# Kernel optimization log

Measured on AMD Instinct MI355X. Metric: run time of the kernel, lower is better.

## Reference

```python
import jax, jax.numpy as jnp
import numpy as np

N, IN_DIM, H1, H2 = 12288, 512, 256, 128

def setup_inputs() -> dict:
    key = jax.random.key(0)
    k = jax.random.split(key, 6)
    glorot = lambda kk, fi, fo: jax.random.normal(kk, (fi, fo), jnp.float32) * np.sqrt(2.0 / (fi + fo))
    return {
        "X": jax.random.normal(k[0], (N, IN_DIM), jnp.float32),
        "adj": jax.random.uniform(k[1], (N, N), jnp.float32) / N,  # scaled like a normalized adjacency
        "noise": jax.random.normal(k[2], (N, H2), jnp.float32),
        "W0": glorot(k[3], IN_DIM, H1),
        "W_mu": glorot(k[4], H1, H2),
        "W_logstd": glorot(k[5], H1, H2),
    }

def reference(X, adj, noise, W0, W_mu, W_logstd):
    # GraphConvSparse layer 1: relu(adj @ (X @ W0))
    hidden = jax.nn.relu(adj @ (X @ W0))            # [N, H1]
    # mean / logstd heads (identity activation)
    mean = adj @ (hidden @ W_mu)                    # [N, H2]
    logstd = adj @ (hidden @ W_logstd)              # [N, H2]
    # reparameterization
    Z = noise * jnp.exp(logstd) + mean              # [N, H2]
    # dot-product decode
    A_pred = jax.nn.sigmoid(Z @ Z.T)                # [N, N]
    return A_pred
```

## Files before the change

kernel.cpp:

```cpp
#include <hip/hip_runtime.h>
#include <stdint.h>

#define NN 12288
#define IND 512
#define H1D 256
#define H2D 128

using bf16x8 = __attribute__((ext_vector_type(8))) short;
using f32x4  = __attribute__((ext_vector_type(4))) float;

__device__ __forceinline__ unsigned short f2bf(float f){
  unsigned int u = __float_as_uint(f);
  return (unsigned short)((u + 0x7fffu + ((u >> 16) & 1u)) >> 16);
}
__device__ __forceinline__ float bf2f(unsigned short h){
  return __uint_as_float(((unsigned int)h) << 16);
}
__device__ __forceinline__ void gload_lds16(const void* g, void* l){
  __builtin_amdgcn_global_load_lds(
      (const __attribute__((address_space(1))) unsigned int*)(uintptr_t)g,
      (__attribute__((address_space(3))) unsigned int*)(unsigned int)(uintptr_t)l,
      16, 0, 0);
}

__global__ __launch_bounds__(256) void k_xw0(const float* __restrict__ X,
                                             const float* __restrict__ W0,
                                             unsigned short* __restrict__ XW0T){
  __shared__ float XsT[32][68];
  __shared__ float Ws[32][36];
  const int t  = (int)threadIdx.x;
  const int n0 = (int)blockIdx.x * 64;
  const int h0 = (int)blockIdx.y * 32;
  const int xr = t >> 2, xc = (t & 3) * 8;
  const int h  = t >> 3, ng = t & 7;
  float acc[8];
#pragma unroll
  for (int j = 0; j < 8; ++j) acc[j] = 0.f;

  for (int k0 = 0; k0 < IND; k0 += 32){
    {
      const float* xp = X + (size_t)(n0 + xr) * IND + k0 + xc;
      float4 a = *(const float4*)xp;
      float4 b = *(const float4*)(xp + 4);
      XsT[xc+0][xr]=a.x; XsT[xc+1][xr]=a.y; XsT[xc+2][xr]=a.z; XsT[xc+3][xr]=a.w;
      XsT[xc+4][xr]=b.x; XsT[xc+5][xr]=b.y; XsT[xc+6][xr]=b.z; XsT[xc+7][xr]=b.w;
    }
    if (t < 128){
      const float* wp = W0 + (size_t)(k0 + xr) * H1D + h0 + xc;
      float4 a = *(const float4*)wp;
      float4 b = *(const float4*)(wp + 4);
      Ws[xr][xc+0]=a.x; Ws[xr][xc+1]=a.y; Ws[xr][xc+2]=a.z; Ws[xr][xc+3]=a.w;
      Ws[xr][xc+4]=b.x; Ws[xr][xc+5]=b.y; Ws[xr][xc+6]=b.z; Ws[xr][xc+7]=b.w;
    }
    __syncthreads();
#pragma unroll 8
    for (int kk = 0; kk < 32; ++kk){
      float wv = Ws[kk][h];
      const float4 x0 = *(const float4*)&XsT[kk][ng*8];
      const float4 x1 = *(const float4*)&XsT[kk][ng*8+4];
      acc[0] += x0.x*wv; acc[1] += x0.y*wv; acc[2] += x0.z*wv; acc[3] += x0.w*wv;
      acc[4] += x1.x*wv; acc[5] += x1.y*wv; acc[6] += x1.z*wv; acc[7] += x1.w*wv;
    }
    __syncthreads();
  }
  uint4 pk;
  pk.x = (unsigned)f2bf(acc[0]) | ((unsigned)f2bf(acc[1]) << 16);
  pk.y = (unsigned)f2bf(acc[2]) | ((unsigned)f2bf(acc[3]) << 16);
  pk.z = (unsigned)f2bf(acc[4]) | ((unsigned)f2bf(acc[5]) << 16);
  pk.w = (unsigned)f2bf(acc[6]) | ((unsigned)f2bf(acc[7]) << 16);
  *(uint4*)(XW0T + (size_t)(h0 + h) * NN + n0 + ng*8) = pk;
}

__global__ __launch_bounds__(512, 4) void k_gemm_adj(const float* __restrict__ A,
                                                     const unsigned short* __restrict__ Bt,
                                                     float* __restrict__ part){
  __shared__ unsigned short Alds[2][48*64];
  __shared__ unsigned short Blds[2][256*64];
  const int t = (int)threadIdx.x;
  const int w = t >> 6, l = t & 63;
  const int l15 = l & 15, l16 = l >> 4;
  const int m0 = (int)blockIdx.x * 48;
  const int khalf = (int)blockIdx.y;
  const int kbase = khalf * 6144;
  const size_t kbyte = (size_t)kbase * 2;

  f32x4 acc[3][2];
#pragma unroll
  for (int mi = 0; mi < 3; ++mi)
#pragma unroll
    for (int ni = 0; ni < 2; ++ni) acc[mi][ni] = 0;

  const int ar = t >> 3, ac8 = (t & 7) * 8;
  const bool astage = (t < 384);
  const float* abase = A + (size_t)(m0 + ar) * NN + kbase + ac8;
  const int aoff = ar*128 + ((ac8*2) ^ ((ar & 7) << 4));

  if (astage){
    float4 v0 = *(const float4*)(abase);
    float4 v1 = *(const float4*)(abase + 4);
    uint4 pk;
    pk.x = (unsigned)f2bf(v0.x) | ((unsigned)f2bf(v0.y) << 16);
    pk.y = (unsigned)f2bf(v0.z) | ((unsigned)f2bf(v0.w) << 16);
    pk.z = (unsigned)f2bf(v1.x) | ((unsigned)f2bf(v1.y) << 16);
    pk.w = (unsigned)f2bf(v1.z) | ((unsigned)f2bf(v1.w) << 16);
    *(uint4*)((char*)Alds[0] + aoff) = pk;
  }
#pragma unroll
  for (int i = 0; i < 4; ++i){
    int P = i*8192 + t*16;
    int row = P >> 7;
    int Li = (P & 127) ^ ((row & 7) << 4);
    gload_lds16((const char*)Bt + (size_t)row * (NN*2) + kbyte + Li,
                (char*)Blds[0] + i*8192 + w*1024);
  }
  __syncthreads();

  for (int s = 0; s < 96; ++s){
    const int cur = s & 1, nxt = cur ^ 1;
    float4 v0, v1;
    if (s + 1 < 96){
      if (astage){
        v0 = *(const float4*)(abase + (size_t)(s+1)*64);
        v1 = *(const float4*)(abase + (size_t)(s+1)*64 + 4);
      }
#pragma unroll
      for (int i = 0; i < 4; ++i){
        int P = i*8192 + t*16;
        int row = P >> 7;
        int Li = (P & 127) ^ ((row & 7) << 4);
        gload_lds16((const char*)Bt + (size_t)row * (NN*2) + kbyte + (size_t)(s+1)*128 + Li,
                    (char*)Blds[nxt] + i*8192 + w*1024);
      }
    }
#pragma unroll
    for (int kk = 0; kk < 2; ++kk){
      bf16x8 af[3], bfr[2];
#pragma unroll
      for (int mi = 0; mi < 3; ++mi){
        int row = mi*16 + l15;
        int off = row*128 + ((kk*64 + l16*16) ^ ((row & 7) << 4));
        af[mi] = *(const bf16x8*)((const char*)Alds[cur] + off);
      }
#pragma unroll
      for (int ni = 0; ni < 2; ++ni){
        int row = w*32 + ni*16 + l15;
        int off = row*128 + ((kk*64 + l16*16) ^ ((row & 7) << 4));
        bfr[ni] = *(const bf16x8*)((const char*)Blds[cur] + off);
      }
#pragma unroll
      for (int mi = 0; mi < 3; ++mi)
#pragma unroll
        for (int ni = 0; ni < 2; ++ni)
          acc[mi][ni] = __builtin_amdgcn_mfma_f32_16x16x32_bf16(af[mi], bfr[ni], acc[mi][ni], 0, 0, 0);
    }
    if (s + 1 < 96 && astage){
      uint4 pk;
      pk.x = (unsigned)f2bf(v0.x) | ((unsigned)f2bf(v0.y) << 16);
      pk.y = (unsigned)f2bf(v0.z) | ((unsigned)f2bf(v0.w) << 16);
      pk.z = (unsigned)f2bf(v1.x) | ((unsigned)f2bf(v1.y) << 16);
      pk.w = (unsigned)f2bf(v1.z) | ((unsigned)f2bf(v1.w) << 16);
      *(uint4*)((char*)Alds[nxt] + aoff) = pk;
    }
    __syncthreads();
  }

  float* P = part + (size_t)khalf * NN * H1D;
#pragma unroll
  for (int mi = 0; mi < 3; ++mi)
#pragma unroll
    for (int ni = 0; ni < 2; ++ni){
      int gr = m0 + mi*16 + l16*4;
      int gc = w*32 + ni*16 + l15;
#pragma unroll
      for (int v = 0; v < 4; ++v)
        P[(size_t)(gr + v) * H1D + gc] = acc[mi][ni][v];
    }
}

__global__ __launch_bounds__(256) void k_combine_ht(const float* __restrict__ p0,
                                                    const float* __restrict__ p1,
                                                    unsigned short* __restrict__ HT){
  __shared__ float Ls[64][65];
  const int t = (int)threadIdx.x;
  const int n0 = (int)blockIdx.x * 64;
  const int h0 = (int)blockIdx.y * 64;
  const int lr = t >> 4, lc = (t & 15) * 4;
#pragma unroll
  for (int q = 0; q < 4; ++q){
    int n = lr + q*16;
    size_t idx = (size_t)(n0 + n) * H1D + h0 + lc;
    float4 a = *(const float4*)(p0 + idx);
    float4 b = *(const float4*)(p1 + idx);
    Ls[n][lc+0] = fmaxf(a.x + b.x, 0.f);
    Ls[n][lc+1] = fmaxf(a.y + b.y, 0.f);
    Ls[n][lc+2] = fmaxf(a.z + b.z, 0.f);
    Ls[n][lc+3] = fmaxf(a.w + b.w, 0.f);
  }
  __syncthreads();
  const int hr = t >> 2, nc = (t & 3) * 16;
  unsigned int pk[8];
#pragma unroll
  for (int q = 0; q < 8; ++q){
    float x0 = Ls[nc + q*2 + 0][hr];
    float x1 = Ls[nc + q*2 + 1][hr];
    pk[q] = (unsigned)f2bf(x0) | ((unsigned)f2bf(x1) << 16);
  }
  unsigned short* dst = HT + (size_t)(h0 + hr) * NN + n0 + nc;
  *(uint4*)(dst)     = *(uint4*)&pk[0];
  *(uint4*)(dst + 8) = *(uint4*)&pk[4];
}

__global__ __launch_bounds__(256) void k_heads(const float* __restrict__ p0,
                                               const float* __restrict__ Wmu,
                                               const float* __restrict__ Wls,
                                               const float* __restrict__ noise,
                                               unsigned short* __restrict__ Zhi,
                                               unsigned short* __restrict__ Zlo){
  __shared__ float AHs[32][256];
  __shared__ float Wms[32][128];
  __shared__ float Wlss[32][128];
  const float* p1 = p0 + (size_t)NN * H1D;
  const int t  = (int)threadIdx.x;
  const int r0 = (int)blockIdx.x * 32;
  {
    const int r = t >> 3, c0 = (t & 7) * 32;
    size_t base = (size_t)(r0 + r) * H1D + c0;
#pragma unroll
    for (int q = 0; q < 8; ++q){
      float4 a = *(const float4*)(p0 + base + q*4);
      float4 b = *(const float4*)(p1 + base + q*4);
      AHs[r][c0 + q*4 + 0] = a.x + b.x;
      AHs[r][c0 + q*4 + 1] = a.y + b.y;
      AHs[r][c0 + q*4 + 2] = a.z + b.z;
      AHs[r][c0 + q*4 + 3] = a.w + b.w;
    }
  }
  const int j = t & 127, rg = t >> 7;
  float mu[16], ls[16];
#pragma unroll
  for (int r = 0; r < 16; ++r){ mu[r] = 0.f; ls[r] = 0.f; }

  for (int kc = 0; kc < 8; ++kc){
    __syncthreads();
    {
      const int r = t >> 3, c0 = (t & 7) * 16;
      const float* pm = Wmu + (size_t)(kc*32 + r) * H2D + c0;
      const float* pl = Wls + (size_t)(kc*32 + r) * H2D + c0;
#pragma unroll
      for (int q = 0; q < 4; ++q){
        *(float4*)&Wms[r][c0 + q*4]  = *(const float4*)(pm + q*4);
        *(float4*)&Wlss[r][c0 + q*4] = *(const float4*)(pl + q*4);
      }
    }
    __syncthreads();
#pragma unroll 4
    for (int k = 0; k < 32; ++k){
      float wm = Wms[k][j], wl = Wlss[k][j];
#pragma unroll
      for (int r = 0; r < 16; ++r){
        float a = AHs[rg*16 + r][kc*32 + k];
        mu[r] += a * wm;
        ls[r] += a * wl;
      }
    }
  }
#pragma unroll
  for (int r = 0; r < 16; ++r){
    const int i = r0 + rg*16 + r;
    float z = noise[(size_t)i * H2D + j] * __expf(ls[r]) + mu[r];
    unsigned short zh = f2bf(z);
    unsigned short zl = f2bf(z - bf2f(zh));
    Zhi[(size_t)i * H2D + j] = zh;
    Zlo[(size_t)i * H2D + j] = zl;
  }
}

__global__ __launch_bounds__(512) void k_decode(const unsigned short* __restrict__ Zhi,
                                                const unsigned short* __restrict__ Zlo,
                                                float* __restrict__ Out){
  __shared__ unsigned short T[4][128*64];
  const int t = (int)threadIdx.x;
  const int w = t >> 6, l = t & 63;
  const int l15 = l & 15, l16 = l >> 4;
  const int wr = w >> 2, wc = w & 3;
  const size_t m0 = (size_t)blockIdx.x * 128;
  const size_t n0 = (size_t)blockIdx.y * 128;

  f32x4 acc[4][2];
#pragma unroll
  for (int mi = 0; mi < 4; ++mi)
#pragma unroll
    for (int ni = 0; ni < 2; ++ni) acc[mi][ni] = 0;

#pragma unroll
  for (int p = 0; p < 2; ++p){
    if (p) __syncthreads();
#pragma unroll
    for (int i = 0; i < 2; ++i){
      int P = i*8192 + t*16;
      int row = P >> 7;
      int Li = (P & 127) ^ ((row & 7) << 4);
      size_t ga = (size_t)row * 256 + (size_t)p * 128 + Li;
      char* lb0 = (char*)T[0] + i*8192 + w*1024;
      char* lb1 = (char*)T[1] + i*8192 + w*1024;
      char* lb2 = (char*)T[2] + i*8192 + w*1024;
      char* lb3 = (char*)T[3] + i*8192 + w*1024;
      gload_lds16((const char*)Zhi + m0*256 + ga, lb0);
      gload_lds16((const char*)Zlo + m0*256 + ga, lb1);
      gload_lds16((const char*)Zhi + n0*256 + ga, lb2);
      gload_lds16((const char*)Zlo + n0*256 + ga, lb3);
    }
    __syncthreads();
#pragma unroll
    for (int kk = 0; kk < 2; ++kk){
      bf16x8 ah[4], al[4], bh[2], bl[2];
#pragma unroll
      for (int mi = 0; mi < 4; ++mi){
        int row = wr*64 + mi*16 + l15;
        int off = row*128 + ((kk*64 + l16*16) ^ ((row & 7) << 4));
        ah[mi] = *(const bf16x8*)((const char*)T[0] + off);
        al[mi] = *(const bf16x8*)((const char*)T[1] + off);
      }
#pragma unroll
      for (int ni = 0; ni < 2; ++ni){
        int row = wc*32 + ni*16 + l15;
        int off = row*128 + ((kk*64 + l16*16) ^ ((row & 7) << 4));
        bh[ni] = *(const bf16x8*)((const char*)T[2] + off);
        bl[ni] = *(const bf16x8*)((const char*)T[3] + off);
      }
#pragma unroll
      for (int mi = 0; mi < 4; ++mi)
#pragma unroll
        for (int ni = 0; ni < 2; ++ni){
          acc[mi][ni] = __builtin_amdgcn_mfma_f32_16x16x32_bf16(ah[mi], bh[ni], acc[mi][ni], 0, 0, 0);
          acc[mi][ni] = __builtin_amdgcn_mfma_f32_16x16x32_bf16(ah[mi], bl[ni], acc[mi][ni], 0, 0, 0);
          acc[mi][ni] = __builtin_amdgcn_mfma_f32_16x16x32_bf16(al[mi], bh[ni], acc[mi][ni], 0, 0, 0);
        }
    }
  }

#pragma unroll
  for (int mi = 0; mi < 4; ++mi)
#pragma unroll
    for (int ni = 0; ni < 2; ++ni){
      size_t gr = m0 + (size_t)(wr*64 + mi*16 + l16*4);
      size_t gc = n0 + (size_t)(wc*32 + ni*16 + l15);
#pragma unroll
      for (int v = 0; v < 4; ++v){
        float x = acc[mi][ni][v];
        Out[(gr + v) * (size_t)NN + gc] = 1.0f / (1.0f + __expf(-x));
      }
    }
}

extern "C" void kernel_launch(void* const* d_in, const int* in_sizes, int n_in,
                              void* d_out, int out_size, void* d_ws, size_t ws_size,
                              hipStream_t stream) {
  const float* X     = (const float*)d_in[0];
  const float* adj   = (const float*)d_in[1];
  const float* noise = (const float*)d_in[2];
  const float* W0    = (const float*)d_in[3];
  const float* Wmu   = (const float*)d_in[4];
  const float* Wls   = (const float*)d_in[5];
  float* out = (float*)d_out;
  char* ws = (char*)d_ws;

  unsigned short* XW0T = (unsigned short*)(ws);
  unsigned short* HT   = (unsigned short*)(ws + 6291456);
  unsigned short* Zhi  = (unsigned short*)(ws + 12582912);
  unsigned short* Zlo  = (unsigned short*)(ws + 15728640);
  float* part = (ws_size >= (size_t)18874368 + 25165824)
              ? (float*)(ws + 18874368) : (float*)d_out;

  k_xw0<<<dim3(192, 8), 256, 0, stream>>>(X, W0, XW0T);
  k_gemm_adj<<<dim3(256, 2), 512, 0, stream>>>(adj, XW0T, part);
  k_combine_ht<<<dim3(192, 4), 256, 0, stream>>>(part, part + (size_t)NN * H1D, HT);
  k_gemm_adj<<<dim3(256, 2), 512, 0, stream>>>(adj, HT, part);
  k_heads<<<384, 256, 0, stream>>>(part, Wmu, Wls, noise, Zhi, Zlo);
  k_decode<<<dim3(96, 96), 512, 0, stream>>>(Zhi, Zlo, out);
}
```

Measured before the change: 723.2 us.

## Generalize adj GEMM with deeper A prefetch, MFMA for X@W0, nontemporal IO

Replaces the scalar FP32 X@W0 kernel with a W0 transpose kernel plus the shared MFMA bf16 GEMM template, which writes transposed bf16 output directly. The adjacency GEMM main loop is unrolled by two, with A register prefetch two stages ahead and explicit waitcnt/barrier control so global loads of the streamed fp32 adjacency overlap more MFMA work. A loads and decode sigmoid stores use nontemporal hints to avoid polluting cache. This adds register pressure and relies on hand-placed waitcnt being correct.

```diff
diff --git a/kernel.cpp b/kernel.cpp
--- a/kernel.cpp
+++ b/kernel.cpp
@@ -22,58 +22,85 @@
       (__attribute__((address_space(3))) unsigned int*)(unsigned int)(uintptr_t)l,
       16, 0, 0);
 }
-
-__global__ __launch_bounds__(256) void k_xw0(const float* __restrict__ X,
-                                             const float* __restrict__ W0,
-                                             unsigned short* __restrict__ XW0T){
-  __shared__ float XsT[32][68];
-  __shared__ float Ws[32][36];
-  const int t  = (int)threadIdx.x;
-  const int n0 = (int)blockIdx.x * 64;
-  const int h0 = (int)blockIdx.y * 32;
-  const int xr = t >> 2, xc = (t & 3) * 8;
-  const int h  = t >> 3, ng = t & 7;
-  float acc[8];
-#pragma unroll
-  for (int j = 0; j < 8; ++j) acc[j] = 0.f;
-
-  for (int k0 = 0; k0 < IND; k0 += 32){
-    {
-      const float* xp = X + (size_t)(n0 + xr) * IND + k0 + xc;
-      float4 a = *(const float4*)xp;
-      float4 b = *(const float4*)(xp + 4);
-      XsT[xc+0][xr]=a.x; XsT[xc+1][xr]=a.y; XsT[xc+2][xr]=a.z; XsT[xc+3][xr]=a.w;
-      XsT[xc+4][xr]=b.x; XsT[xc+5][xr]=b.y; XsT[xc+6][xr]=b.z; XsT[xc+7][xr]=b.w;
-    }
-    if (t < 128){
-      const float* wp = W0 + (size_t)(k0 + xr) * H1D + h0 + xc;
-      float4 a = *(const float4*)wp;
-      float4 b = *(const float4*)(wp + 4);
-      Ws[xr][xc+0]=a.x; Ws[xr][xc+1]=a.y; Ws[xr][xc+2]=a.z; Ws[xr][xc+3]=a.w;
-      Ws[xr][xc+4]=b.x; Ws[xr][xc+5]=b.y; Ws[xr][xc+6]=b.z; Ws[xr][xc+7]=b.w;
-    }
-    __syncthreads();
-#pragma unroll 8
-    for (int kk = 0; kk < 32; ++kk){
-      float wv = Ws[kk][h];
-      const float4 x0 = *(const float4*)&XsT[kk][ng*8];
-      const float4 x1 = *(const float4*)&XsT[kk][ng*8+4];
-      acc[0] += x0.x*wv; acc[1] += x0.y*wv; acc[2] += x0.z*wv; acc[3] += x0.w*wv;
-      acc[4] += x1.x*wv; acc[5] += x1.y*wv; acc[6] += x1.z*wv; acc[7] += x1.w*wv;
-    }
-    __syncthreads();
-  }
+__device__ __forceinline__ uint4 pack_bf8(f32x4 lo, f32x4 hi){
   uint4 pk;
-  pk.x = (unsigned)f2bf(acc[0]) | ((unsigned)f2bf(acc[1]) << 16);
-  pk.y = (unsigned)f2bf(acc[2]) | ((unsigned)f2bf(acc[3]) << 16);
-  pk.z = (unsigned)f2bf(acc[4]) | ((unsigned)f2bf(acc[5]) << 16);
-  pk.w = (unsigned)f2bf(acc[6]) | ((unsigned)f2bf(acc[7]) << 16);
-  *(uint4*)(XW0T + (size_t)(h0 + h) * NN + n0 + ng*8) = pk;
-}
-
-__global__ __launch_bounds__(512, 4) void k_gemm_adj(const float* __restrict__ A,
-                                                     const unsigned short* __restrict__ Bt,
-                                                     float* __restrict__ part){
+  pk.x = (unsigned)f2bf(lo[0]) | ((unsigned)f2bf(lo[1]) << 16);
+  pk.y = (unsigned)f2bf(lo[2]) | ((unsigned)f2bf(lo[3]) << 16);
+  pk.z = (unsigned)f2bf(hi[0]) | ((unsigned)f2bf(hi[1]) << 16);
+  pk.w = (unsigned)f2bf(hi[2]) | ((unsigned)f2bf(hi[3]) << 16);
+  return pk;
+}
+__device__ __forceinline__ void step_sync(bool deep){
+  if (deep) asm volatile("s_waitcnt vmcnt(2) lgkmcnt(0)" ::: "memory");
+  else      asm volatile("s_waitcnt vmcnt(0) lgkmcnt(0)" ::: "memory");
+  __builtin_amdgcn_s_barrier();
+  __builtin_amdgcn_sched_barrier(0);
+}
+
+__global__ __launch_bounds__(256) void k_w0t(const float* __restrict__ W0,
+                                             unsigned short* __restrict__ W0T){
+  __shared__ float Ls[64][65];
+  const int t = (int)threadIdx.x;
+  const int k0 = (int)blockIdx.x * 64;
+  const int h0 = (int)blockIdx.y * 64;
+  {
+    const int r = t >> 2, c = (t & 3) * 16;
+    const float* p = W0 + (size_t)(k0 + r) * H1D + h0 + c;
+#pragma unroll
+    for (int q = 0; q < 4; ++q)
+      *(float4*)&Ls[r][c + q*4] = *(const float4*)(p + q*4);
+  }
+  __syncthreads();
+  const int h = t >> 2, kc = (t & 3) * 16;
+  unsigned int pk[8];
+#pragma unroll
+  for (int q = 0; q < 8; ++q){
+    float x0 = Ls[kc + q*2 + 0][h];
+    float x1 = Ls[kc + q*2 + 1][h];
+    pk[q] = (unsigned)f2bf(x0) | ((unsigned)f2bf(x1) << 16);
+  }
+  unsigned short* dst = W0T + (size_t)(h0 + h) * IND + k0 + kc;
+  *(uint4*)(dst)     = *(uint4*)&pk[0];
+  *(uint4*)(dst + 8) = *(uint4*)&pk[4];
+}
+
+#define GEMM_MFMA(CUR) \
+  { _Pragma("unroll") \
+    for (int kk = 0; kk < 2; ++kk){ \
+      bf16x8 af[3], bfr[2]; \
+      _Pragma("unroll") \
+      for (int mi = 0; mi < 3; ++mi){ \
+        int row = mi*16 + l15; \
+        int off = row*128 + ((kk*64 + l16*16) ^ ((row & 7) << 4)); \
+        af[mi] = *(const bf16x8*)((const char*)Alds[CUR] + off); \
+      } \
+      _Pragma("unroll") \
+      for (int ni = 0; ni < 2; ++ni){ \
+        int row = w*32 + ni*16 + l15; \
+        int off = row*128 + ((kk*64 + l16*16) ^ ((row & 7) << 4)); \
+        bfr[ni] = *(const bf16x8*)((const char*)Blds[CUR] + off); \
+      } \
+      _Pragma("unroll") \
+      for (int mi = 0; mi < 3; ++mi) \
+        _Pragma("unroll") \
+        for (int ni = 0; ni < 2; ++ni) \
+          acc[mi][ni] = __builtin_amdgcn_mfma_f32_16x16x32_bf16(af[mi], bfr[ni], acc[mi][ni], 0, 0, 0); \
+    } }
+
+#define GLDS_B(SIDX, BUF) \
+  { _Pragma("unroll") \
+    for (int i = 0; i < 4; ++i){ \
+      int P = i*8192 + t*16; \
+      int row = P >> 7; \
+      int Li = (P & 127) ^ ((row & 7) << 4); \
+      gload_lds16(btb + (size_t)row * btsb + kbyte + (size_t)(SIDX)*128 + Li, \
+                  (char*)Blds[BUF] + i*8192 + w*1024); \
+    } }
+
+template<int MODE, bool RELU>
+__global__ __launch_bounds__(512, 4) void k_gemm(const float* __restrict__ A, int lda, int K,
+                                                 const unsigned short* __restrict__ Bt, int bt_stride_e,
+                                                 void* __restrict__ Out){
   __shared__ unsigned short Alds[2][48*64];
   __shared__ unsigned short Blds[2][256*64];
   const int t = (int)threadIdx.x;
@@ -81,8 +108,11 @@
   const int l15 = l & 15, l16 = l >> 4;
   const int m0 = (int)blockIdx.x * 48;
   const int khalf = (int)blockIdx.y;
-  const int kbase = khalf * 6144;
+  const int kbase = khalf * K;
   const size_t kbyte = (size_t)kbase * 2;
+  const size_t btsb = (size_t)bt_stride_e * 2;
+  const char* btb = (const char*)Bt;
+  const int S = K >> 6;
 
   f32x4 acc[3][2];
 #pragma unroll
@@ -92,89 +122,76 @@
 
   const int ar = t >> 3, ac8 = (t & 7) * 8;
   const bool astage = (t < 384);
-  const float* abase = A + (size_t)(m0 + ar) * NN + kbase + ac8;
+  const float* abase = A + (size_t)(m0 + ar) * lda + kbase + ac8;
   const int aoff = ar*128 + ((ac8*2) ^ ((ar & 7) << 4));
 
+  f32x4 a0l, a0h, a1l, a1h;
   if (astage){
-    float4 v0 = *(const float4*)(abase);
-    float4 v1 = *(const float4*)(abase + 4);
-    uint4 pk;
-    pk.x = (unsigned)f2bf(v0.x) | ((unsigned)f2bf(v0.y) << 16);
-    pk.y = (unsigned)f2bf(v0.z) | ((unsigned)f2bf(v0.w) << 16);
-    pk.z = (unsigned)f2bf(v1.x) | ((unsigned)f2bf(v1.y) << 16);
-    pk.w = (unsigned)f2bf(v1.z) | ((unsigned)f2bf(v1.w) << 16);
-    *(uint4*)((char*)Alds[0] + aoff) = pk;
-  }
-#pragma unroll
-  for (int i = 0; i < 4; ++i){
-    int P = i*8192 + t*16;
-    int row = P >> 7;
-    int Li = (P & 127) ^ ((row & 7) << 4);
-    gload_lds16((const char*)Bt + (size_t)row * (NN*2) + kbyte + Li,
-                (char*)Blds[0] + i*8192 + w*1024);
-  }
+    const f32x4* p0 = (const f32x4*)abase;
+    a0l = __builtin_nontemporal_load(p0);
+    a0h = __builtin_nontemporal_load(p0 + 1);
+    const f32x4* p1 = (const f32x4*)(abase + 64);
+    a1l = __builtin_nontemporal_load(p1);
+    a1h = __builtin_nontemporal_load(p1 + 1);
+  }
+  GLDS_B(0, 0);
+  if (astage) *(uint4*)((char*)Alds[0] + aoff) = pack_bf8(a0l, a0h);
   __syncthreads();
 
-  for (int s = 0; s < 96; ++s){
-    const int cur = s & 1, nxt = cur ^ 1;
-    float4 v0, v1;
-    if (s + 1 < 96){
-      if (astage){
-        v0 = *(const float4*)(abase + (size_t)(s+1)*64);
-        v1 = *(const float4*)(abase + (size_t)(s+1)*64 + 4);
-      }
-#pragma unroll
-      for (int i = 0; i < 4; ++i){
-        int P = i*8192 + t*16;
-        int row = P >> 7;
-        int Li = (P & 127) ^ ((row & 7) << 4);
-        gload_lds16((const char*)Bt + (size_t)row * (NN*2) + kbyte + (size_t)(s+1)*128 + Li,
-                    (char*)Blds[nxt] + i*8192 + w*1024);
-      }
-    }
-#pragma unroll
-    for (int kk = 0; kk < 2; ++kk){
-      bf16x8 af[3], bfr[2];
-#pragma unroll
-      for (int mi = 0; mi < 3; ++mi){
-        int row = mi*16 + l15;
-        int off = row*128 + ((kk*64 + l16*16) ^ ((row & 7) << 4));
-        af[mi] = *(const bf16x8*)((const char*)Alds[cur] + off);
-      }
+  for (int s = 0; s < S; s += 2){
+    if (s + 1 < S) GLDS_B(s + 1, 1);
+    if (astage && s + 2 < S){
+      const f32x4* p = (const f32x4*)(abase + (size_t)(s + 2) * 64);
+      a0l = __builtin_nontemporal_load(p);
+      a0h = __builtin_nontemporal_load(p + 1);
+    }
+    GEMM_MFMA(0);
+    if (astage && s + 1 < S)
+      *(uint4*)((char*)Alds[1] + aoff) = pack_bf8(a1l, a1h);
+    if (s + 1 < S) step_sync(astage && (s + 2 < S));
+    if (s + 1 < S){
+      if (s + 2 < S) GLDS_B(s + 2, 0);
+      if (astage && s + 3 < S){
+        const f32x4* p = (const f32x4*)(abase + (size_t)(s + 3) * 64);
+        a1l = __builtin_nontemporal_load(p);
+        a1h = __builtin_nontemporal_load(p + 1);
+      }
+      GEMM_MFMA(1);
+      if (astage && s + 2 < S)
+        *(uint4*)((char*)Alds[0] + aoff) = pack_bf8(a0l, a0h);
+      if (s + 2 < S) step_sync(astage);
+    }
+  }
+
+  if (MODE == 0){
+    unsigned short* HT = (unsigned short*)Out;
+#pragma unroll
+    for (int mi = 0; mi < 3; ++mi)
 #pragma unroll
       for (int ni = 0; ni < 2; ++ni){
-        int row = w*32 + ni*16 + l15;
-        int off = row*128 + ((kk*64 + l16*16) ^ ((row & 7) << 4));
-        bfr[ni] = *(const bf16x8*)((const char*)Blds[cur] + off);
-      }
-#pragma unroll
-      for (int mi = 0; mi < 3; ++mi)
-#pragma unroll
-        for (int ni = 0; ni < 2; ++ni)
-          acc[mi][ni] = __builtin_amdgcn_mfma_f32_16x16x32_bf16(af[mi], bfr[ni], acc[mi][ni], 0, 0, 0);
-    }
-    if (s + 1 < 96 && astage){
-      uint4 pk;
-      pk.x = (unsigned)f2bf(v0.x) | ((unsigned)f2bf(v0.y) << 16);
-      pk.y = (unsigned)f2bf(v0.z) | ((unsigned)f2bf(v0.w) << 16);
-      pk.z = (unsigned)f2bf(v1.x) | ((unsigned)f2bf(v1.y) << 16);
-      pk.w = (unsigned)f2bf(v1.z) | ((unsigned)f2bf(v1.w) << 16);
-      *(uint4*)((char*)Alds[nxt] + aoff) = pk;
-    }
-    __syncthreads();
-  }
-
-  float* P = part + (size_t)khalf * NN * H1D;
-#pragma unroll
-  for (int mi = 0; mi < 3; ++mi)
-#pragma unroll
-    for (int ni = 0; ni < 2; ++ni){
-      int gr = m0 + mi*16 + l16*4;
-      int gc = w*32 + ni*16 + l15;
-#pragma unroll
-      for (int v = 0; v < 4; ++v)
-        P[(size_t)(gr + v) * H1D + gc] = acc[mi][ni][v];
-    }
+        int gr = m0 + mi*16 + l16*4;
+        int gc = w*32 + ni*16 + l15;
+        float x0 = acc[mi][ni][0], x1 = acc[mi][ni][1];
+        float x2 = acc[mi][ni][2], x3 = acc[mi][ni][3];
+        if (RELU){ x0 = fmaxf(x0,0.f); x1 = fmaxf(x1,0.f); x2 = fmaxf(x2,0.f); x3 = fmaxf(x3,0.f); }
+        uint2 pk;
+        pk.x = (unsigned)f2bf(x0) | ((unsigned)f2bf(x1) << 16);
+        pk.y = (unsigned)f2bf(x2) | ((unsigned)f2bf(x3) << 16);
+        *(uint2*)(HT + (size_t)gc * NN + gr) = pk;
+      }
+  } else {
+    float* P = (float*)Out + (size_t)khalf * NN * H1D;
+#pragma unroll
+    for (int mi = 0; mi < 3; ++mi)
+#pragma unroll
+      for (int ni = 0; ni < 2; ++ni){
+        int gr = m0 + mi*16 + l16*4;
+        int gc = w*32 + ni*16 + l15;
+#pragma unroll
+        for (int v = 0; v < 4; ++v)
+          P[(size_t)(gr + v) * H1D + gc] = acc[mi][ni][v];
+      }
+  }
 }
 
 __global__ __launch_bounds__(256) void k_combine_ht(const float* __restrict__ p0,
@@ -348,7 +365,8 @@
 #pragma unroll
       for (int v = 0; v < 4; ++v){
         float x = acc[mi][ni][v];
-        Out[(gr + v) * (size_t)NN + gc] = 1.0f / (1.0f + __expf(-x));
+        float sg = 1.0f / (1.0f + __expf(-x));
+        __builtin_nontemporal_store(sg, &Out[(gr + v) * (size_t)NN + gc]);
       }
     }
 }
@@ -369,13 +387,15 @@
   unsigned short* HT   = (unsigned short*)(ws + 6291456);
   unsigned short* Zhi  = (unsigned short*)(ws + 12582912);
   unsigned short* Zlo  = (unsigned short*)(ws + 15728640);
-  float* part = (ws_size >= (size_t)18874368 + 25165824)
-              ? (float*)(ws + 18874368) : (float*)d_out;
-
-  k_xw0<<<dim3(192, 8), 256, 0, stream>>>(X, W0, XW0T);
-  k_gemm_adj<<<dim3(256, 2), 512, 0, stream>>>(adj, XW0T, part);
+  unsigned short* W0T  = (unsigned short*)(ws + 18874368);
+  float* part = (ws_size >= (size_t)19136512 + 25165824)
+              ? (float*)(ws + 19136512) : (float*)d_out;
+
+  k_w0t<<<dim3(8, 4), 256, 0, stream>>>(W0, W0T);
+  k_gemm<0,false><<<dim3(256, 1), 512, 0, stream>>>(X, IND, IND, W0T, IND, (void*)XW0T);
+  k_gemm<1,false><<<dim3(256, 2), 512, 0, stream>>>(adj, NN, 6144, XW0T, NN, (void*)part);
   k_combine_ht<<<dim3(192, 4), 256, 0, stream>>>(part, part + (size_t)NN * H1D, HT);
-  k_gemm_adj<<<dim3(256, 2), 512, 0, stream>>>(adj, HT, part);
+  k_gemm<1,false><<<dim3(256, 2), 512, 0, stream>>>(adj, NN, 6144, HT, NN, (void*)part);
   k_heads<<<384, 256, 0, stream>>>(part, Wmu, Wls, noise, Zhi, Zlo);
   k_decode<<<dim3(96, 96), 512, 0, stream>>>(Zhi, Zlo, out);
 }
```

New measurement: 718.8 us. No clear change (-0.6%).
